# Performance work log

Hardware: AMD Instinct MI355X
Metric: run time of the kernel (lower is better)

Reference implementation:

```python
import jax, jax.numpy as jnp
import numpy as np

N = 100000
E = 1000000
IN_F, HID, NCLS = 128, 128, 40
EPS = 1e-5


def _gconv(h, src, dst, W, b):
    # DGL GraphConv with norm='both', allow_zero_in_degree=True (degrees clamped to >=1).
    ones = jnp.ones(src.shape, jnp.float32)
    dout = jnp.clip(jax.ops.segment_sum(ones, src, num_segments=N), 1.0)   # out-degree of src nodes
    din = jnp.clip(jax.ops.segment_sum(ones, dst, num_segments=N), 1.0)    # in-degree of dst nodes
    x = (h * jax.lax.rsqrt(dout)[:, None]) @ W            # [N, out] matmul-first (linear commutes with sum-aggregation)
    y = jax.ops.segment_sum(x[src], dst, num_segments=N)  # SpMM: scatter-add over edges
    y = y * jax.lax.rsqrt(din)[:, None]
    return y + b if b is not None else y


def _bn(h, gamma, beta):
    # BatchNorm1d training-mode math over the node dimension (biased variance).
    m = jnp.mean(h, axis=0)
    v = jnp.mean(jnp.square(h - m), axis=0)
    return (h - m) * jax.lax.rsqrt(v + EPS) * gamma + beta


def setup_inputs() -> dict:
    key = jax.random.key(0)
    ks = jax.random.split(key, 16)
    feat = jax.random.normal(ks[0], (N, IN_F), jnp.float32)
    src0 = jax.random.randint(ks[1], (E,), 0, N, jnp.int32)
    dst0 = jax.random.randint(ks[2], (E,), 0, N, jnp.int32)
    src1 = jax.random.randint(ks[3], (E,), 0, N, jnp.int32)
    dst1 = jax.random.randint(ks[4], (E,), 0, N, jnp.int32)
    order_attn = jax.random.uniform(ks[5], (2,), jnp.float32)
    s = lambda d_in, d_out: 1.0 / np.sqrt(d_in)
    W0 = jax.random.uniform(ks[6], (IN_F, HID), jnp.float32, -s(IN_F, HID), s(IN_F, HID))
    W1 = jax.random.uniform(ks[7], (HID, HID), jnp.float32, -s(HID, HID), s(HID, HID))
    W2 = jax.random.uniform(ks[8], (HID, NCLS), jnp.float32, -s(HID, NCLS), s(HID, NCLS))
    b2 = jnp.zeros((NCLS,), jnp.float32)
    L0 = jax.random.uniform(ks[9], (IN_F, HID), jnp.float32, -s(IN_F, HID), s(IN_F, HID))
    L1 = jax.random.uniform(ks[10], (HID, HID), jnp.float32, -s(HID, HID), s(HID, HID))
    L2 = jax.random.uniform(ks[11], (HID, NCLS), jnp.float32, -s(HID, NCLS), s(HID, NCLS))
    gamma0 = jnp.ones((HID,), jnp.float32); beta0 = jnp.zeros((HID,), jnp.float32)
    gamma1 = jnp.ones((HID,), jnp.float32); beta1 = jnp.zeros((HID,), jnp.float32)
    return dict(feat=feat, src0=src0, dst0=dst0, src1=src1, dst1=dst1, order_attn=order_attn,
                W0=W0, W1=W1, W2=W2, b2=b2, L0=L0, L1=L1, L2=L2,
                gamma0=gamma0, beta0=beta0, gamma1=gamma1, beta1=beta1)


def reference(feat, src0, dst0, src1, dst1, order_attn, W0, W1, W2, b2, L0, L1, L2,
              gamma0, beta0, gamma1, beta1):
    # Multi-graph path (len(graph)==2, n_layers==3, use_linear=True); dropout = identity (eval).
    h = feat
    # layer 0: order_attn-weighted combination of two adjacency variants
    conv1 = _gconv(h, src0, dst0, W0, None)
    conv2 = _gconv(h, src1, dst1, W0, None)
    conv = order_attn[0] * conv1 + order_attn[1] * conv2
    h = conv + h @ L0
    h = jax.nn.relu(_bn(h, gamma0, beta0))
    # layer 1 (convs[-2]) on graph[0]
    h = _gconv(h, src0, dst0, W1, None) + h @ L1
    h = jax.nn.relu(_bn(h, gamma1, beta1))
    # layer 2 (convs[-1]) on graph[0], with bias
    h = _gconv(h, src0, dst0, W2, b2) + h @ L2
    return h
```

## Files before the change

kernel.cpp:

```cpp
#include <hip/hip_runtime.h>
#include <math.h>

#define N_NODES 100000
#define N_EDGES 1000000
#define F 128
#define NC 40
#define BN_EPS 1e-5f
#define CH 64
#define EC (N_EDGES / CH)
#define WIN0 65536
#define NB1 (N_NODES - WIN0)
#define PROW (N_NODES / 4)
#define CSU 68
#define GB 1563
#define X2S 32

typedef unsigned int uint;
typedef unsigned short ushort;
typedef __attribute__((ext_vector_type(8))) short vbf8;
typedef __attribute__((ext_vector_type(4))) float vf4;

__device__ __forceinline__ float bf_lo(uint v) { return __uint_as_float(v << 16); }
__device__ __forceinline__ float bf_hi(uint v) { return __uint_as_float(v & 0xffff0000u); }
__device__ __forceinline__ ushort f2bf(float f) {
  uint u = __float_as_uint(f);
  u = u + 0x7fffu + ((u >> 16) & 1u);
  return (ushort)(u >> 16);
}
__device__ __forceinline__ uint pk2(float a, float b) {
  return (uint)f2bf(a) | ((uint)f2bf(b) << 16);
}

__global__ __launch_bounds__(256) void hist_count_k(
    const int* __restrict__ s0, const int* __restrict__ d0,
    const int* __restrict__ s1, const int* __restrict__ d1,
    unsigned* __restrict__ partial) {
  __shared__ unsigned bins[16384];
  int c = blockIdx.x, w = blockIdx.y, a = blockIdx.z;
  const int* keys = (a == 0) ? s0 : (a == 1) ? d0 : (a == 2) ? s1 : d1;
  int base = w * WIN0;
  int nb = w ? NB1 : WIN0;
  int nwords = nb >> 2;
  int t = threadIdx.x;
  for (int i = t; i < nwords; i += 256) bins[i] = 0;
  __syncthreads();
  int e0 = c * EC;
  for (int e = e0 + t; e < e0 + EC; e += 256) {
    int b = keys[e] - base;
    if ((unsigned)b < (unsigned)nb)
      atomicAdd(&bins[b >> 2], 1u << ((b & 3) * 8));
  }
  __syncthreads();
  unsigned* dst = partial + (size_t)(a * CH + c) * PROW + (w ? (WIN0 >> 2) : 0);
  for (int i = t; i < nwords; i += 256) dst[i] = bins[i];
}

__global__ __launch_bounds__(256) void deg_reduce_k(
    unsigned* __restrict__ partial, float* __restrict__ rs4, ushort* __restrict__ rsO01u,
    int* __restrict__ degIn0, int* __restrict__ degIn1) {
  int word = blockIdx.x * 256 + threadIdx.x;
  if (word >= PROW) return;
  int a = blockIdx.y;
  bool din = (a == 1) || (a == 3);
  unsigned r0 = 0, r1 = 0, r2 = 0, r3 = 0;
  unsigned* rowp = partial + (size_t)a * CH * PROW + word;
  for (int c = 0; c < CH; ++c) {
    unsigned* p = rowp + (size_t)c * PROW;
    unsigned v = *p;
    if (din) *p = r0 | (r1 << 8) | (r2 << 16) | (r3 << 24);
    r0 += v & 255u; r1 += (v >> 8) & 255u; r2 += (v >> 16) & 255u; r3 += (v >> 24) & 255u;
  }
  int b = word * 4;
  float4 r;
  r.x = rsqrtf((float)max(r0, 1u));
  r.y = rsqrtf((float)max(r1, 1u));
  r.z = rsqrtf((float)max(r2, 1u));
  r.w = rsqrtf((float)max(r3, 1u));
  *(float4*)&rs4[(size_t)a * N_NODES + b] = r;
  if (a == 0) {
    rsO01u[2 * (b + 0)] = f2bf(r.x); rsO01u[2 * (b + 1)] = f2bf(r.y);
    rsO01u[2 * (b + 2)] = f2bf(r.z); rsO01u[2 * (b + 3)] = f2bf(r.w);
  }
  if (a == 2) {
    rsO01u[2 * (b + 0) + 1] = f2bf(r.x); rsO01u[2 * (b + 1) + 1] = f2bf(r.y);
    rsO01u[2 * (b + 2) + 1] = f2bf(r.z); rsO01u[2 * (b + 3) + 1] = f2bf(r.w);
  }
  if (a == 1) { degIn0[b] = r0; degIn0[b + 1] = r1; degIn0[b + 2] = r2; degIn0[b + 3] = r3; }
  if (a == 3) { degIn1[b] = r0; degIn1[b + 1] = r1; degIn1[b + 2] = r2; degIn1[b + 3] = r3; }
}

__global__ void scan_local_k(const int* __restrict__ cnt0, const int* __restrict__ cnt1,
                             int* __restrict__ out0, int* __restrict__ out1,
                             int* __restrict__ bsum) {
  __shared__ int lds[256];
  const int* cnt = blockIdx.y ? cnt1 : cnt0;
  int* out = blockIdx.y ? out1 : out0;
  int base = blockIdx.x * 2048;
  int t = threadIdx.x;
  int v[8];
  int s = 0;
#pragma unroll
  for (int j = 0; j < 8; ++j) {
    int idx = base + t * 8 + j;
    v[j] = (idx < N_NODES) ? cnt[idx] : 0;
    s += v[j];
  }
  lds[t] = s;
  __syncthreads();
  for (int off = 1; off < 256; off <<= 1) {
    int x = (t >= off) ? lds[t - off] : 0;
    __syncthreads();
    lds[t] += x;
    __syncthreads();
  }
  int excl = lds[t] - s;
  if (t == 255) bsum[blockIdx.y * 64 + blockIdx.x] = lds[255];
  int run = excl;
#pragma unroll
  for (int j = 0; j < 8; ++j) {
    int idx = base + t * 8 + j;
    if (idx < N_NODES) out[idx] = run;
    run += v[j];
  }
}

__global__ void scan_top_k(int* bsum, int nb) {
  int w = threadIdx.x >> 6, t = threadIdx.x & 63;
  int* b = bsum + w * 64;
  int orig = (t < nb) ? b[t] : 0;
  int v = orig;
  for (int off = 1; off < 64; off <<= 1) {
    int u = __shfl_up(v, off);
    if (t >= off) v += u;
  }
  if (t < nb) b[t] = v - orig;
}

__global__ void scan_apply_k(int* __restrict__ rp0, int* __restrict__ rp1,
                             const int* __restrict__ bsum) {
  int* rp = blockIdx.y ? rp1 : rp0;
  const int* bs = bsum + blockIdx.y * 64;
  int i = blockIdx.x * 256 + threadIdx.x;
  if (i < N_NODES) rp[i] += bs[i >> 11];
  if (i == 0) rp[N_NODES] = N_EDGES;
}

__global__ __launch_bounds__(256) void csr_fill2_k(
    const int* __restrict__ src0, const int* __restrict__ dst0, const int* __restrict__ rp0g,
    int* __restrict__ csr0g,
    const int* __restrict__ src1, const int* __restrict__ dst1, const int* __restrict__ rp1g,
    int* __restrict__ csr1g, const unsigned* __restrict__ partial) {
  __shared__ unsigned bins[16384];
  int c = blockIdx.x, w = blockIdx.y, g = blockIdx.z;
  const int* src = g ? src1 : src0;
  const int* dst = g ? dst1 : dst0;
  const int* rp = g ? rp1g : rp0g;
  int* csr = g ? csr1g : csr0g;
  int aIdx = g ? 3 : 1;
  int base = w * WIN0;
  int nb = w ? NB1 : WIN0;
  int nwords = nb >> 2;
  const unsigned* sp = partial + (size_t)(aIdx * CH + c) * PROW + (w ? (WIN0 >> 2) : 0);
  int t = threadIdx.x;
  for (int i = t; i < nwords; i += 256) bins[i] = sp[i];
  __syncthreads();
  int e0 = c * EC;
  for (int e = e0 + t; e < e0 + EC; e += 256) {
    int d = dst[e];
    int b = d - base;
    if ((unsigned)b < (unsigned)nb) {
      int sh = (b & 3) * 8;
      unsigned old = atomicAdd(&bins[b >> 2], 1u << sh);
      int off = (old >> sh) & 255;
      csr[rp[d] + off] = src[e];
    }
  }
}

__global__ __launch_bounds__(256) void pack_all_k(
    const float* __restrict__ x, uint* __restrict__ y,
    const float* __restrict__ Wa, const float* __restrict__ Wb,
    const float* __restrict__ Wc, const float* __restrict__ Wd,
    ushort* __restrict__ pk) {
  int b = blockIdx.x;
  int t = threadIdx.x;
  if (b < 1024) {
    size_t total = (size_t)N_NODES * F / 8;
    for (size_t idx = b * 256 + t; idx < total; idx += (size_t)1024 * 256) {
      float4 v1 = ((const float4*)x)[idx * 2];
      float4 v2 = ((const float4*)x)[idx * 2 + 1];
      uint4 o;
      o.x = pk2(v1.x, v1.y);
      o.y = pk2(v1.z, v1.w);
      o.z = pk2(v2.x, v2.y);
      o.w = pk2(v2.z, v2.w);
      ((uint4*)y)[idx] = o;
    }
  } else {
    int bb = b - 1024;
    int m = bb >> 3;
    int idx = (bb & 7) * 256 + t;
    const float* W = (m == 0) ? Wa : (m == 1) ? Wb : (m == 2) ? Wc : Wd;
    int lane = idx & 63;
    int nt = (idx >> 6) & 7;
    int ks = idx >> 9;
    int j = (lane & 15) + nt * 16;
    int kb = (lane >> 4) * 8 + ks * 32;
    ushort v[8];
#pragma unroll
    for (int q = 0; q < 8; ++q) v[q] = f2bf(W[(size_t)(kb + q) * F + j]);
    *(uint4*)(pk + (size_t)m * 16384 + (size_t)idx * 8) = *(uint4*)v;
  }
}

__global__ void st_part_k(const float* __restrict__ stm, float* __restrict__ stp, int ncopies) {
  int b = blockIdx.x, t = threadIdx.x;
  int lo = b * 25, hi = min(ncopies, lo + 25);
  float s = 0.f;
  for (int k = lo; k < hi; ++k) s += stm[(size_t)k * 256 + t];
  stp[b * 256 + t] = s;
}

__global__ void st_final_k(const float* __restrict__ stp, float* __restrict__ st) {
  int t = threadIdx.x;
  float s = 0.f;
#pragma unroll
  for (int k = 0; k < 64; ++k) s += stp[k * 256 + t];
  st[t] = s;
}

__device__ __forceinline__ void acc8(uint4 v, float c, float* a) {
  a[0] = fmaf(bf_lo(v.x), c, a[0]); a[1] = fmaf(bf_hi(v.x), c, a[1]);
  a[2] = fmaf(bf_lo(v.y), c, a[2]); a[3] = fmaf(bf_hi(v.y), c, a[3]);
  a[4] = fmaf(bf_lo(v.z), c, a[4]); a[5] = fmaf(bf_hi(v.z), c, a[5]);
  a[6] = fmaf(bf_lo(v.w), c, a[6]); a[7] = fmaf(bf_hi(v.w), c, a[7]);
}

__device__ __forceinline__ void gather_run(const int* __restrict__ p, int n, float w,
                                           const float* __restrict__ rsO,
                                           const uint4* __restrict__ xr, int l, float* a) {
  int e = 0;
  for (; e + 3 < n; e += 4) {
    int s0 = p[e], s1 = p[e + 1], s2 = p[e + 2], s3 = p[e + 3];
    float c0 = w * rsO[s0], c1 = w * rsO[s1];
    float c2 = w * rsO[s2], c3 = w * rsO[s3];
    uint4 v0 = xr[(size_t)s0 * 16 + l];
    uint4 v1 = xr[(size_t)s1 * 16 + l];
    uint4 v2 = xr[(size_t)s2 * 16 + l];
    uint4 v3 = xr[(size_t)s3 * 16 + l];
    acc8(v0, c0, a); acc8(v1, c1, a); acc8(v2, c2, a); acc8(v3, c3, a);
  }
  for (; e < n; ++e) {
    int s = p[e];
    float c = w * rsO[s];
    uint4 v = xr[(size_t)s * 16 + l];
    acc8(v, c, a);
  }
}

__global__ __launch_bounds__(256) void gather_dual_q_k(
    const uint* __restrict__ xbf, const float* __restrict__ attn,
    const float* __restrict__ rsO0f, const float* __restrict__ rsO1f,
    const float* __restrict__ rsI0, const int* __restrict__ rp0, const int* __restrict__ csr0,
    const float* __restrict__ rsI1, const int* __restrict__ rp1, const int* __restrict__ csr1,
    uint* __restrict__ outbf) {
  int node = blockIdx.x * 16 + (threadIdx.x >> 4);
  int l = threadIdx.x & 15;
  int b0 = rp0[node], n0 = rp0[node + 1] - b0;
  int b1 = rp1[node], n1 = rp1[node + 1] - b1;
  float w0 = attn[0] * rsI0[node];
  float w1 = attn[1] * rsI1[node];
  const uint4* xr = (const uint4*)xbf;
  float a[8] = {0.f, 0.f, 0.f, 0.f, 0.f, 0.f, 0.f, 0.f};
  gather_run(csr0 + b0, n0, w0, rsO0f, xr, l, a);
  gather_run(csr1 + b1, n1, w1, rsO1f, xr, l, a);
  uint4 o;
  o.x = pk2(a[0], a[1]); o.y = pk2(a[2], a[3]);
  o.z = pk2(a[4], a[5]); o.w = pk2(a[6], a[7]);
  ((uint4*)outbf)[(size_t)node * 16 + l] = o;
}

__device__ __forceinline__ void accbn(uint4 v, float c, const float* sc, const float* sh,
                                      float* a) {
  a[0] = fmaf(fmaxf(fmaf(bf_lo(v.x), sc[0], sh[0]), 0.f), c, a[0]);
  a[1] = fmaf(fmaxf(fmaf(bf_hi(v.x), sc[1], sh[1]), 0.f), c, a[1]);
  a[2] = fmaf(fmaxf(fmaf(bf_lo(v.y), sc[2], sh[2]), 0.f), c, a[2]);
  a[3] = fmaf(fmaxf(fmaf(bf_hi(v.y), sc[3], sh[3]), 0.f), c, a[3]);
  a[4] = fmaf(fmaxf(fmaf(bf_lo(v.z), sc[4], sh[4]), 0.f), c, a[4]);
  a[5] = fmaf(fmaxf(fmaf(bf_hi(v.z), sc[5], sh[5]), 0.f), c, a[5]);
  a[6] = fmaf(fmaxf(fmaf(bf_lo(v.w), sc[6], sh[6]), 0.f), c, a[6]);
  a[7] = fmaf(fmaxf(fmaf(bf_hi(v.w), sc[7], sh[7]), 0.f), c, a[7]);
}

__global__ __launch_bounds__(256) void gather_bn_q_k(
    const uint* __restrict__ xbf, const float* __restrict__ st,
    const float* __restrict__ gamma, const float* __restrict__ beta,
    const float* __restrict__ rsO,
    const float* __restrict__ rsI, const int* __restrict__ rp, const int* __restrict__ csr,
    uint* __restrict__ outbf) {
  int node = blockIdx.x * 16 + (threadIdx.x >> 4);
  int l = threadIdx.x & 15;
  float sc[8], sh[8];
#pragma unroll
  for (int j = 0; j < 8; ++j) {
    int c = 8 * l + j;
    float m = st[c] * (1.f / (float)N_NODES);
    float v = st[128 + c] * (1.f / (float)N_NODES) - m * m;
    float s = gamma[c] * rsqrtf(fmaxf(v, 0.f) + BN_EPS);
    sc[j] = s;
    sh[j] = beta[c] - m * s;
  }
  int b0 = rp[node], T = rp[node + 1] - b0;
  const int* p = csr + b0;
  const uint4* xr = (const uint4*)xbf;
  float a[8] = {0.f, 0.f, 0.f, 0.f, 0.f, 0.f, 0.f, 0.f};
  int e = 0;
  for (; e + 1 < T; e += 2) {
    int s0 = p[e], s1 = p[e + 1];
    float c0 = rsO[s0], c1 = rsO[s1];
    uint4 v0 = xr[(size_t)s0 * 16 + l];
    uint4 v1 = xr[(size_t)s1 * 16 + l];
    accbn(v0, c0, sc, sh, a);
    accbn(v1, c1, sc, sh, a);
  }
  if (e < T) {
    int s0 = p[e];
    float c0 = rsO[s0];
    uint4 v0 = xr[(size_t)s0 * 16 + l];
    accbn(v0, c0, sc, sh, a);
  }
  float sd = rsI[node];
  uint4 o;
  o.x = pk2(a[0] * sd, a[1] * sd); o.y = pk2(a[2] * sd, a[3] * sd);
  o.z = pk2(a[4] * sd, a[5] * sd); o.w = pk2(a[6] * sd, a[7] * sd);
  ((uint4*)outbf)[(size_t)node * 16 + l] = o;
}

__global__ void gather40_add_k(const uint* __restrict__ x2bf, const float* __restrict__ rsI,
                               const int* __restrict__ rp, const int* __restrict__ csr,
                               float* __restrict__ out) {
  int node = (blockIdx.x * 256 + threadIdx.x) >> 5;
  int lane = threadIdx.x & 31;
  if (node >= N_NODES || lane >= 20) return;
  float l = 0.f, h = 0.f;
  int e = rp[node], end = rp[node + 1];
  for (; e + 3 < end; e += 4) {
    int sA = csr[e], sB = csr[e + 1], sC = csr[e + 2], sD = csr[e + 3];
    uint vA = x2bf[(size_t)sA * X2S + lane];
    uint vB = x2bf[(size_t)sB * X2S + lane];
    uint vC = x2bf[(size_t)sC * X2S + lane];
    uint vD = x2bf[(size_t)sD * X2S + lane];
    l += (bf_lo(vA) + bf_lo(vB)) + (bf_lo(vC) + bf_lo(vD));
    h += (bf_hi(vA) + bf_hi(vB)) + (bf_hi(vC) + bf_hi(vD));
  }
  for (; e < end; ++e) {
    uint vA = x2bf[(size_t)csr[e] * X2S + lane];
    l += bf_lo(vA);
    h += bf_hi(vA);
  }
  float sd = rsI[node];
  float2 p = *(float2*)(out + (size_t)node * NC + lane * 2);
  *(float2*)(out + (size_t)node * NC + lane * 2) = make_float2(p.x + l * sd, p.y + h * sd);
}

__global__ __launch_bounds__(256) void gemm_mfma_k(
    const ushort* __restrict__ A1, const ushort* __restrict__ A2,
    const ushort* __restrict__ pkA, const ushort* __restrict__ pkB,
    float* __restrict__ stm, ushort* __restrict__ Cb) {
  __shared__ uint Cl[64 * CSU];
  __shared__ float sst[256];
  int t = threadIdx.x;
  sst[t] = 0.f;
  __syncthreads();
  int wave = t >> 6, lane = t & 63;
  int kgrp = lane >> 4, lrow = lane & 15;
  int arow = blockIdx.x * 64 + wave * 16 + lrow;
  bool rok = arow < N_NODES;
  const vbf8* a1p = (const vbf8*)(A1 + (size_t)(rok ? arow : 0) * F);
  const vbf8* a2p = (const vbf8*)(A2 + (size_t)(rok ? arow : 0) * F);
  const vbf8* wap = (const vbf8*)pkA + lane;
  const vbf8* wbp = (const vbf8*)pkB + lane;
  vbf8 zero = {0, 0, 0, 0, 0, 0, 0, 0};
  vf4 acc[8];
#pragma unroll
  for (int i = 0; i < 8; ++i) acc[i] = (vf4){0.f, 0.f, 0.f, 0.f};
#pragma unroll
  for (int ks = 0; ks < 4; ++ks) {
    vbf8 a1 = rok ? a1p[ks * 4 + kgrp] : zero;
    vbf8 a2 = rok ? a2p[ks * 4 + kgrp] : zero;
#pragma unroll
    for (int nt = 0; nt < 8; ++nt)
      acc[nt] = __builtin_amdgcn_mfma_f32_16x16x32_bf16(a1, wap[(ks * 8 + nt) * 64], acc[nt], 0, 0, 0);
#pragma unroll
    for (int nt = 0; nt < 8; ++nt)
      acc[nt] = __builtin_amdgcn_mfma_f32_16x16x32_bf16(a2, wbp[(ks * 8 + nt) * 64], acc[nt], 0, 0, 0);
  }
  int row_l = wave * 16 + kgrp * 4;
#pragma unroll
  for (int nt = 0; nt < 8; ++nt) {
#pragma unroll
    for (int r = 0; r < 4; ++r) {
      float w = acc[nt][r];
      float o = __shfl_xor(w, 1);
      if ((lrow & 1) == 0) Cl[(row_l + r) * CSU + nt * 8 + (lrow >> 1)] = pk2(w, o);
    }
  }
#pragma unroll
  for (int nt = 0; nt < 8; ++nt) {
    float s = acc[nt][0] + acc[nt][1] + acc[nt][2] + acc[nt][3];
    float q = acc[nt][0] * acc[nt][0] + acc[nt][1] * acc[nt][1] +
              acc[nt][2] * acc[nt][2] + acc[nt][3] * acc[nt][3];
    s += __shfl_xor(s, 16); q += __shfl_xor(q, 16);
    s += __shfl_xor(s, 32); q += __shfl_xor(q, 32);
    if (lane < 16) {
      atomicAdd(&sst[nt * 16 + lane], s);
      atomicAdd(&sst[128 + nt * 16 + lane], q);
    }
  }
  __syncthreads();
#pragma unroll
  for (int i = 0; i < 4; ++i) {
    int u = t + 256 * i;
    int row = u >> 4, seg = (u & 15) * 4;
    int grow = blockIdx.x * 64 + row;
    if (grow < N_NODES)
      *(uint4*)((uint*)Cb + (size_t)grow * 64 + seg) = *(uint4*)&Cl[row * CSU + seg];
  }
  stm[(size_t)blockIdx.x * 256 + t] = sst[t];
}

__global__ __launch_bounds__(256) void gemm_mfma_bn_k(
    const ushort* __restrict__ A1, const ushort* __restrict__ A2,
    const float* __restrict__ stin, const float* __restrict__ gamma,
    const float* __restrict__ beta,
    const ushort* __restrict__ pkA, const ushort* __restrict__ pkB,
    float* __restrict__ stm, ushort* __restrict__ Cb) {
  __shared__ uint Cl[64 * CSU];
  __shared__ float sst[256];
  __shared__ float scl[128], shl[128];
  int t = threadIdx.x;
  sst[t] = 0.f;
  if (t < 128) {
    float m = stin[t] * (1.f / (float)N_NODES);
    float v = stin[128 + t] * (1.f / (float)N_NODES) - m * m;
    float s = gamma[t] * rsqrtf(fmaxf(v, 0.f) + BN_EPS);
    scl[t] = s;
    shl[t] = beta[t] - m * s;
  }
  __syncthreads();
  int wave = t >> 6, lane = t & 63;
  int kgrp = lane >> 4, lrow = lane & 15;
  int arow = blockIdx.x * 64 + wave * 16 + lrow;
  bool rok = arow < N_NODES;
  const vbf8* a1p = (const vbf8*)(A1 + (size_t)(rok ? arow : 0) * F);
  const vbf8* a2p = (const vbf8*)(A2 + (size_t)(rok ? arow : 0) * F);
  const vbf8* wap = (const vbf8*)pkA + lane;
  const vbf8* wbp = (const vbf8*)pkB + lane;
  vbf8 zero = {0, 0, 0, 0, 0, 0, 0, 0};
  vf4 acc[8];
#pragma unroll
  for (int i = 0; i < 8; ++i) acc[i] = (vf4){0.f, 0.f, 0.f, 0.f};
#pragma unroll
  for (int ks = 0; ks < 4; ++ks) {
    vbf8 a1 = rok ? a1p[ks * 4 + kgrp] : zero;
    vbf8 a2 = zero;
    if (rok) {
      vbf8 a2r = a2p[ks * 4 + kgrp];
      const float* scp = &scl[ks * 32 + kgrp * 8];
      const float* shp = &shl[ks * 32 + kgrp * 8];
      ushort o[8];
#pragma unroll
      for (int q = 0; q < 8; ++q) {
        float f = __uint_as_float(((uint)(ushort)a2r[q]) << 16);
        f = fmaxf(fmaf(f, scp[q], shp[q]), 0.f);
        o[q] = f2bf(f);
      }
      a2 = *(vbf8*)o;
    }
#pragma unroll
    for (int nt = 0; nt < 8; ++nt)
      acc[nt] = __builtin_amdgcn_mfma_f32_16x16x32_bf16(a1, wap[(ks * 8 + nt) * 64], acc[nt], 0, 0, 0);
#pragma unroll
    for (int nt = 0; nt < 8; ++nt)
      acc[nt] = __builtin_amdgcn_mfma_f32_16x16x32_bf16(a2, wbp[(ks * 8 + nt) * 64], acc[nt], 0, 0, 0);
  }
  int row_l = wave * 16 + kgrp * 4;
#pragma unroll
  for (int nt = 0; nt < 8; ++nt) {
#pragma unroll
    for (int r = 0; r < 4; ++r) {
      float w = acc[nt][r];
      float o = __shfl_xor(w, 1);
      if ((lrow & 1) == 0) Cl[(row_l + r) * CSU + nt * 8 + (lrow >> 1)] = pk2(w, o);
    }
  }
#pragma unroll
  for (int nt = 0; nt < 8; ++nt) {
    float s = acc[nt][0] + acc[nt][1] + acc[nt][2] + acc[nt][3];
    float q = acc[nt][0] * acc[nt][0] + acc[nt][1] * acc[nt][1] +
              acc[nt][2] * acc[nt][2] + acc[nt][3] * acc[nt][3];
    s += __shfl_xor(s, 16); q += __shfl_xor(q, 16);
    s += __shfl_xor(s, 32); q += __shfl_xor(q, 32);
    if (lane < 16) {
      atomicAdd(&sst[nt * 16 + lane], s);
      atomicAdd(&sst[128 + nt * 16 + lane], q);
    }
  }
  __syncthreads();
#pragma unroll
  for (int i = 0; i < 4; ++i) {
    int u = t + 256 * i;
    int row = u >> 4, seg = (u & 15) * 4;
    int grow = blockIdx.x * 64 + row;
    if (grow < N_NODES)
      *(uint4*)((uint*)Cb + (size_t)grow * 64 + seg) = *(uint4*)&Cl[row * CSU + seg];
  }
  stm[(size_t)blockIdx.x * 256 + t] = sst[t];
}

__global__ __launch_bounds__(256) void gemm40_dual_k(
    const uint* __restrict__ h1b, const float* __restrict__ st,
    const float* __restrict__ gamma, const float* __restrict__ beta,
    const float* __restrict__ W2, const float* __restrict__ L2, const float* __restrict__ bias,
    const float* __restrict__ rsO, uint* __restrict__ x2bf, float* __restrict__ outp) {
  __shared__ float Alds[25 * 128];
  __shared__ float Wl[128 * NC];
  __shared__ float Ll[128 * NC];
  __shared__ float scl[128], shl[128];
  int t = threadIdx.x;
  int r0 = blockIdx.x * 25;
  if (t < 128) {
    float m = st[t] / (float)N_NODES;
    float v = st[128 + t] / (float)N_NODES - m * m;
    float s = gamma[t] * rsqrtf(fmaxf(v, 0.f) + BN_EPS);
    scl[t] = s;
    shl[t] = beta[t] - m * s;
  }
  __syncthreads();
#pragma unroll
  for (int p = 0; p < 4; ++p) {
    int flat = t * 4 + p * 1024;
    if (flat < 25 * 128) {
      int lrr = flat >> 7, k = flat & 127;
      int row = r0 + lrr;
      float4 v = make_float4(0.f, 0.f, 0.f, 0.f);
      if (row < N_NODES) {
        uint2 u = *(const uint2*)(h1b + (size_t)row * 64 + (k >> 1));
        v = make_float4(bf_lo(u.x), bf_hi(u.x), bf_lo(u.y), bf_hi(u.y));
      }
      float4 scv = *(float4*)&scl[k];
      float4 shv = *(float4*)&shl[k];
      v.x = fmaxf(fmaf(v.x, scv.x, shv.x), 0.f);
      v.y = fmaxf(fmaf(v.y, scv.y, shv.y), 0.f);
      v.z = fmaxf(fmaf(v.z, scv.z, shv.z), 0.f);
      v.w = fmaxf(fmaf(v.w, scv.w, shv.w), 0.f);
      *(float4*)&Alds[flat] = v;
    }
  }
#pragma unroll
  for (int p = 0; p < 5; ++p) {
    int flat = t * 4 + p * 1024;
    if (flat < 128 * NC) {
      *(float4*)&Wl[flat] = *(const float4*)(W2 + flat);
      *(float4*)&Ll[flat] = *(const float4*)(L2 + flat);
    }
  }
  __syncthreads();
  if (t < 250) {
    int lrr = t / 10, cg = t % 10;
    float w0 = 0.f, w1 = 0.f, w2 = 0.f, w3 = 0.f;
    float l0 = 0.f, l1 = 0.f, l2 = 0.f, l3 = 0.f;
#pragma unroll 8
    for (int k = 0; k < 128; ++k) {
      float a = Alds[lrr * 128 + k];
      float4 w = *(float4*)&Wl[k * NC + cg * 4];
      float4 l = *(float4*)&Ll[k * NC + cg * 4];
      w0 = fmaf(a, w.x, w0); w1 = fmaf(a, w.y, w1);
      w2 = fmaf(a, w.z, w2); w3 = fmaf(a, w.w, w3);
      l0 = fmaf(a, l.x, l0); l1 = fmaf(a, l.y, l1);
      l2 = fmaf(a, l.z, l2); l3 = fmaf(a, l.w, l3);
    }
    int row = r0 + lrr;
    if (row < N_NODES) {
      float s = rsO[row];
      uint2 xo = make_uint2(pk2(w0 * s, w1 * s), pk2(w2 * s, w3 * s));
      *(uint2*)(x2bf + (size_t)row * X2S + cg * 2) = xo;
      float4 bv = *(const float4*)(bias + cg * 4);
      float4 oo = make_float4(l0 + bv.x, l1 + bv.y, l2 + bv.z, l3 + bv.w);
      *(float4*)(outp + (size_t)row * NC + cg * 4) = oo;
    }
  }
}

extern "C" void kernel_launch(void* const* d_in, const int* in_sizes, int n_in,
                              void* d_out, int out_size, void* d_ws, size_t ws_size,
                              hipStream_t stream) {
  const float* feat = (const float*)d_in[0];
  const int* src0 = (const int*)d_in[1];
  const int* dst0 = (const int*)d_in[2];
  const int* src1 = (const int*)d_in[3];
  const int* dst1 = (const int*)d_in[4];
  const float* attn = (const float*)d_in[5];
  const float* W0 = (const float*)d_in[6];
  const float* W1 = (const float*)d_in[7];
  const float* W2 = (const float*)d_in[8];
  const float* b2 = (const float*)d_in[9];
  const float* L0 = (const float*)d_in[10];
  const float* L1 = (const float*)d_in[11];
  const float* L2 = (const float*)d_in[12];
  const float* gamma0 = (const float*)d_in[13];
  const float* beta0 = (const float*)d_in[14];
  const float* gamma1 = (const float*)d_in[15];
  const float* beta1 = (const float*)d_in[16];
  float* out = (float*)d_out;

  char* base = (char*)d_ws;
  size_t off = 0;
  auto alloc = [&](size_t bytes) -> void* {
    void* p = base + off;
    off += (bytes + 255) & ~(size_t)255;
    return p;
  };
  unsigned* partial = (unsigned*)alloc((size_t)4 * CH * PROW * 4);
  float* rs4 = (float*)alloc(4 * (size_t)N_NODES * 4);
  uint* rsO01 = (uint*)alloc((size_t)N_NODES * 4);
  int* degIn0 = (int*)alloc(N_NODES * 4);
  int* degIn1 = (int*)alloc(N_NODES * 4);
  int* rp0 = (int*)alloc((N_NODES + 1) * 4);
  int* rp1 = (int*)alloc((N_NODES + 1) * 4);
  int* bsum = (int*)alloc(128 * 4);
  int* csr0 = (int*)alloc((size_t)N_EDGES * 4);
  int* csr1 = (int*)alloc((size_t)N_EDGES * 4);
  float* stm0 = (float*)alloc((size_t)GB * 256 * 4);
  float* stm1 = (float*)alloc((size_t)GB * 256 * 4);
  float* stp = (float*)alloc((size_t)64 * 256 * 4);
  float* st0 = (float*)alloc(256 * 4);
  float* st1 = (float*)alloc(256 * 4);
  ushort* wpk = (ushort*)alloc((size_t)4 * 16384 * 2);
  uint* featbf = (uint*)alloc((size_t)N_NODES * 64 * 4);
  uint* aggbf = (uint*)alloc((size_t)N_NODES * 64 * 4);
  uint* hrow = (uint*)alloc((size_t)N_NODES * 64 * 4);
  uint* g1buf = (uint*)alloc((size_t)N_NODES * 64 * 4);
  if (off > ws_size) return;

  uint* x2bf = featbf;

  float* rs_out0 = rs4;
  float* rs_in0 = rs4 + N_NODES;
  float* rs_out1 = rs4 + 2 * N_NODES;
  float* rs_in1 = rs4 + 3 * N_NODES;

  hist_count_k<<<dim3(CH, 2, 4), 256, 0, stream>>>(src0, dst0, src1, dst1, partial);
  deg_reduce_k<<<dim3((PROW + 255) / 256, 4), 256, 0, stream>>>(
      partial, rs4, (ushort*)rsO01, degIn0, degIn1);
  const int SCB = (N_NODES + 2047) / 2048;
  scan_local_k<<<dim3(SCB, 2), 256, 0, stream>>>(degIn0, degIn1, rp0, rp1, bsum);
  scan_top_k<<<1, 128, 0, stream>>>(bsum, SCB);
  scan_apply_k<<<dim3((N_NODES + 255) / 256, 2), 256, 0, stream>>>(rp0, rp1, bsum);
  csr_fill2_k<<<dim3(CH, 2, 2), 256, 0, stream>>>(src0, dst0, rp0, csr0,
                                                  src1, dst1, rp1, csr1, partial);

  pack_all_k<<<1056, 256, 0, stream>>>(feat, featbf, W0, L0, W1, L1, wpk);

  gather_dual_q_k<<<N_NODES / 16, 256, 0, stream>>>(featbf, attn, rs_out0, rs_out1,
                                                    rs_in0, rp0, csr0,
                                                    rs_in1, rp1, csr1, aggbf);
  gemm_mfma_k<<<GB, 256, 0, stream>>>((ushort*)aggbf, (ushort*)featbf, wpk, wpk + 16384,
                                      stm0, (ushort*)hrow);
  st_part_k<<<64, 256, 0, stream>>>(stm0, stp, GB);
  st_final_k<<<1, 256, 0, stream>>>(stp, st0);

  gather_bn_q_k<<<N_NODES / 16, 256, 0, stream>>>(hrow, st0, gamma0, beta0, rs_out0,
                                                  rs_in0, rp0, csr0, g1buf);
  gemm_mfma_bn_k<<<GB, 256, 0, stream>>>((ushort*)g1buf, (ushort*)hrow, st0, gamma0, beta0,
                                         wpk + 2 * 16384, wpk + 3 * 16384, stm1, (ushort*)hrow);
  st_part_k<<<64, 256, 0, stream>>>(stm1, stp, GB);
  st_final_k<<<1, 256, 0, stream>>>(stp, st1);

  gemm40_dual_k<<<(N_NODES + 24) / 25, 256, 0, stream>>>(hrow, st1, gamma1, beta1, W2, L2, b2,
                                                         rs_out0, x2bf, out);
  gather40_add_k<<<(N_NODES * 32 + 255) / 256, 256, 0, stream>>>(x2bf, rs_in0, rp0, csr0, out);
}
```

Baseline: 429.7 us.

## Split CSR fill into eight node windows and fold top-level scan into apply

The CSR fill kernel now splits the node range into eight windows of 12500 nodes instead of two. That shrinks each block's LDS bin array from 64KB to about 12.5KB and launches four times as many blocks, which should raise occupancy and parallelism. The cost is that each edge chunk's dst array is re-read by eight blocks instead of two, so global edge reads grow. Separately, the top-level block-sum scan is computed redundantly inside each scan_apply block, which removes one kernel launch.

```diff
diff --git a/kernel.cpp b/kernel.cpp
--- a/kernel.cpp
+++ b/kernel.cpp
@@ -11,6 +11,8 @@
 #define WIN0 65536
 #define NB1 (N_NODES - WIN0)
 #define PROW (N_NODES / 4)
+#define WIN8 12500
+#define W8W (WIN8 / 4)
 #define CSU 68
 #define GB 1563
 #define X2S 32
@@ -124,51 +126,50 @@
   }
 }
 
-__global__ void scan_top_k(int* bsum, int nb) {
-  int w = threadIdx.x >> 6, t = threadIdx.x & 63;
-  int* b = bsum + w * 64;
-  int orig = (t < nb) ? b[t] : 0;
-  int v = orig;
-  for (int off = 1; off < 64; off <<= 1) {
-    int u = __shfl_up(v, off);
-    if (t >= off) v += u;
-  }
-  if (t < nb) b[t] = v - orig;
-}
-
 __global__ void scan_apply_k(int* __restrict__ rp0, int* __restrict__ rp1,
                              const int* __restrict__ bsum) {
+  __shared__ int ps[64];
   int* rp = blockIdx.y ? rp1 : rp0;
   const int* bs = bsum + blockIdx.y * 64;
-  int i = blockIdx.x * 256 + threadIdx.x;
-  if (i < N_NODES) rp[i] += bs[i >> 11];
+  int t = threadIdx.x;
+  if (t < 64) {
+    int orig = bs[t];
+    int v = orig;
+#pragma unroll
+    for (int off = 1; off < 64; off <<= 1) {
+      int u = __shfl_up(v, off);
+      if (t >= off) v += u;
+    }
+    ps[t] = v - orig;
+  }
+  __syncthreads();
+  int i = blockIdx.x * 256 + t;
+  if (i < N_NODES) rp[i] += ps[i >> 11];
   if (i == 0) rp[N_NODES] = N_EDGES;
 }
 
-__global__ __launch_bounds__(256) void csr_fill2_k(
+__global__ __launch_bounds__(256) void csr_fill8_k(
     const int* __restrict__ src0, const int* __restrict__ dst0, const int* __restrict__ rp0g,
     int* __restrict__ csr0g,
     const int* __restrict__ src1, const int* __restrict__ dst1, const int* __restrict__ rp1g,
     int* __restrict__ csr1g, const unsigned* __restrict__ partial) {
-  __shared__ unsigned bins[16384];
-  int c = blockIdx.x, w = blockIdx.y, g = blockIdx.z;
+  __shared__ unsigned bins[W8W];
+  int w = blockIdx.x, c = blockIdx.y, g = blockIdx.z;
   const int* src = g ? src1 : src0;
   const int* dst = g ? dst1 : dst0;
   const int* rp = g ? rp1g : rp0g;
   int* csr = g ? csr1g : csr0g;
   int aIdx = g ? 3 : 1;
-  int base = w * WIN0;
-  int nb = w ? NB1 : WIN0;
-  int nwords = nb >> 2;
-  const unsigned* sp = partial + (size_t)(aIdx * CH + c) * PROW + (w ? (WIN0 >> 2) : 0);
-  int t = threadIdx.x;
-  for (int i = t; i < nwords; i += 256) bins[i] = sp[i];
+  int base = w * WIN8;
+  const unsigned* sp = partial + (size_t)(aIdx * CH + c) * PROW + (base >> 2);
+  int t = threadIdx.x;
+  for (int i = t; i < W8W; i += 256) bins[i] = sp[i];
   __syncthreads();
   int e0 = c * EC;
   for (int e = e0 + t; e < e0 + EC; e += 256) {
     int d = dst[e];
     int b = d - base;
-    if ((unsigned)b < (unsigned)nb) {
+    if ((unsigned)b < (unsigned)WIN8) {
       int sh = (b & 3) * 8;
       unsigned old = atomicAdd(&bins[b >> 2], 1u << sh);
       int off = (old >> sh) & 255;
@@ -655,9 +656,8 @@
       partial, rs4, (ushort*)rsO01, degIn0, degIn1);
   const int SCB = (N_NODES + 2047) / 2048;
   scan_local_k<<<dim3(SCB, 2), 256, 0, stream>>>(degIn0, degIn1, rp0, rp1, bsum);
-  scan_top_k<<<1, 128, 0, stream>>>(bsum, SCB);
   scan_apply_k<<<dim3((N_NODES + 255) / 256, 2), 256, 0, stream>>>(rp0, rp1, bsum);
-  csr_fill2_k<<<dim3(CH, 2, 2), 256, 0, stream>>>(src0, dst0, rp0, csr0,
+  csr_fill8_k<<<dim3(8, CH, 2), 256, 0, stream>>>(src0, dst0, rp0, csr0,
                                                   src1, dst1, rp1, csr1, partial);
 
   pack_all_k<<<1056, 256, 0, stream>>>(feat, featbf, W0, L0, W1, L1, wpk);
```

Result: no change. 435.5 us (+1.3%).
